# Optimization experiments

Measured on AMD Instinct MI355X. Metric: run time of the kernel, lower is better.

The kernel has to match this reference:

```python
import jax, jax.numpy as jnp
import numpy as np
from jax import lax

BCE_WEIGHT = 0.5
DICE_WEIGHT = 0.5
BOUNDARY_WEIGHT = 3.0
KERNEL_SIZE = 3
SMOOTH = 1e-6
EPS = 1e-7  # clamp for log stability (torch BCE clamps log at -100)


def setup_inputs() -> dict:
    key = jax.random.key(0)
    k1, k2 = jax.random.split(key)
    B, C, H, W = 32, 1, 512, 512
    pred = jax.random.uniform(k1, (B, C, H, W), dtype=jnp.float32)
    target = jax.random.randint(k2, (B, C, H, W), 0, 2, dtype=jnp.int32)
    return {"pred": pred, "target": target}


def _extract_boundary(t):
    # cv2 dilate/erode with all-ones 3x3 kernel == 3x3 max/min pooling.
    # cv2 morphology border behavior (-inf for dilate, +inf for erode)
    # matches reduce_window identity padding with 'SAME'.
    k = KERNEL_SIZE
    win = (1, 1, k, k)
    one = (1, 1, 1, 1)
    dilated = lax.reduce_window(t, -jnp.inf, lax.max, win, one, 'SAME')
    eroded = lax.reduce_window(t, jnp.inf, lax.min, win, one, 'SAME')
    return dilated - eroded  # in {0,1} for binary masks


def reference(pred, target):
    t = target.astype(jnp.float32)  # (B,1,H,W) binary

    # Boundary-aware weighted BCE
    boundary = _extract_boundary(t)
    weights = jnp.where(boundary > 0, BOUNDARY_WEIGHT, 1.0)
    p = jnp.clip(pred, EPS, 1.0 - EPS)
    bce_map = -(t * jnp.log(p) + (1.0 - t) * jnp.log1p(-p))
    bce = jnp.mean(bce_map * weights)

    # Dice loss over flattened tensors
    pf = pred.reshape(-1)
    tf = t.reshape(-1)
    intersection = jnp.sum(pf * tf)
    dice_coef = (2.0 * intersection + SMOOTH) / (jnp.sum(pf) + jnp.sum(tf) + SMOOTH)
    dice = 1.0 - dice_coef

    total = BCE_WEIGHT * bce + DICE_WEIGHT * dice
    return total, bce, dice
```

## Files before the change

### kernel.cpp

```cpp
#include <hip/hip_runtime.h>


#define BB 32
#define HH 512
#define WW 512
#define N_TOTAL (BB * HH * WW)
#define NBLK 2048

__global__ __launch_bounds__(256) void loss_main_kernel(
        const float* __restrict__ pred,
        const int* __restrict__ target,
        float4* __restrict__ partials) {
    const int wave = threadIdx.x >> 6;
    const int lane = threadIdx.x & 63;
    const int gw   = blockIdx.x * 4 + wave;
    const int b    = gw >> 8;
    const int h0   = (gw & 255) << 1;
    const int w0   = lane << 3;

    const size_t img = (size_t)b * (HH * WW);
    const int* tg   = target + img;
    const float* pg = pred + img;

    const int hm = (h0 > 0) ? h0 - 1 : 0;
    const int hp = (h0 + 2 < HH) ? h0 + 2 : HH - 1;

    const int4 r0A = *(const int4*)(tg + (size_t)hm * WW + w0);
    const int4 r0B = *(const int4*)(tg + (size_t)hm * WW + w0 + 4);
    const int4 r1A = *(const int4*)(tg + (size_t)h0 * WW + w0);
    const int4 r1B = *(const int4*)(tg + (size_t)h0 * WW + w0 + 4);
    const int4 r2A = *(const int4*)(tg + (size_t)(h0 + 1) * WW + w0);
    const int4 r2B = *(const int4*)(tg + (size_t)(h0 + 1) * WW + w0 + 4);
    const int4 r3A = *(const int4*)(tg + (size_t)hp * WW + w0);
    const int4 r3B = *(const int4*)(tg + (size_t)hp * WW + w0 + 4);

    const float4 pT0 = *(const float4*)(pg + (size_t)h0 * WW + w0);
    const float4 pT1 = *(const float4*)(pg + (size_t)h0 * WW + w0 + 4);
    const float4 pB0 = *(const float4*)(pg + (size_t)(h0 + 1) * WW + w0);
    const float4 pB1 = *(const float4*)(pg + (size_t)(h0 + 1) * WW + w0 + 4);

#define VC(i, u, c1, c2, d)                                          \
    const int so##i = (c1) | (c2), sa##i = (c1) & (c2);              \
    const int oT##i = so##i | (u), nT##i = sa##i & (u);              \
    const int oB##i = so##i | (d), nB##i = sa##i & (d);
    VC(0, r0A.x, r1A.x, r2A.x, r3A.x)
    VC(1, r0A.y, r1A.y, r2A.y, r3A.y)
    VC(2, r0A.z, r1A.z, r2A.z, r3A.z)
    VC(3, r0A.w, r1A.w, r2A.w, r3A.w)
    VC(4, r0B.x, r1B.x, r2B.x, r3B.x)
    VC(5, r0B.y, r1B.y, r2B.y, r3B.y)
    VC(6, r0B.z, r1B.z, r2B.z, r3B.z)
    VC(7, r0B.w, r1B.w, r2B.w, r3B.w)
#undef VC

    int oTL = __shfl_up(oT7, 1),   nTL = __shfl_up(nT7, 1);
    int oTR = __shfl_down(oT0, 1), nTR = __shfl_down(nT0, 1);
    int oBL = __shfl_up(oB7, 1),   nBL = __shfl_up(nB7, 1);
    int oBR = __shfl_down(oB0, 1), nBR = __shfl_down(nB0, 1);
    if (lane == 0)  { oTL = oT0; nTL = nT0; oBL = oB0; nBL = nB0; }
    if (lane == 63) { oTR = oT7; nTR = nT7; oBR = oB7; nBR = nB7; }

    const int eT0 = (oTL | oT0 | oT1) != (nTL & nT0 & nT1);
    const int eT1 = (oT0 | oT1 | oT2) != (nT0 & nT1 & nT2);
    const int eT2 = (oT1 | oT2 | oT3) != (nT1 & nT2 & nT3);
    const int eT3 = (oT2 | oT3 | oT4) != (nT2 & nT3 & nT4);
    const int eT4 = (oT3 | oT4 | oT5) != (nT3 & nT4 & nT5);
    const int eT5 = (oT4 | oT5 | oT6) != (nT4 & nT5 & nT6);
    const int eT6 = (oT5 | oT6 | oT7) != (nT5 & nT6 & nT7);
    const int eT7 = (oT6 | oT7 | oTR) != (nT6 & nT7 & nTR);
    const int eB0 = (oBL | oB0 | oB1) != (nBL & nB0 & nB1);
    const int eB1 = (oB0 | oB1 | oB2) != (nB0 & nB1 & nB2);
    const int eB2 = (oB1 | oB2 | oB3) != (nB1 & nB2 & nB3);
    const int eB3 = (oB2 | oB3 | oB4) != (nB2 & nB3 & nB4);
    const int eB4 = (oB3 | oB4 | oB5) != (nB3 & nB4 & nB5);
    const int eB5 = (oB4 | oB5 | oB6) != (nB4 & nB5 & nB6);
    const int eB6 = (oB5 | oB6 | oB7) != (nB5 & nB6 & nB7);
    const int eB7 = (oB6 | oB7 | oBR) != (nB6 & nB7 & nBR);

    float wbce = 0.f, inter = 0.f, sp = 0.f;
    int st_i = 0;

#define ACC(T, P, E)                                                   \
    {                                                                  \
        const float pc = fminf(fmaxf((P), 1e-7f), 1.0f - 1e-7f);       \
        const float x  = (T) ? pc : (1.0f - pc);                       \
        wbce += ((E) ? 3.0f : 1.0f) * (-__logf(x));                    \
        sp += (P);                                                     \
        if (T) inter += (P);                                           \
        st_i += (T);                                                   \
    }
    ACC(r1A.x, pT0.x, eT0); ACC(r1A.y, pT0.y, eT1);
    ACC(r1A.z, pT0.z, eT2); ACC(r1A.w, pT0.w, eT3);
    ACC(r1B.x, pT1.x, eT4); ACC(r1B.y, pT1.y, eT5);
    ACC(r1B.z, pT1.z, eT6); ACC(r1B.w, pT1.w, eT7);
    ACC(r2A.x, pB0.x, eB0); ACC(r2A.y, pB0.y, eB1);
    ACC(r2A.z, pB0.z, eB2); ACC(r2A.w, pB0.w, eB3);
    ACC(r2B.x, pB1.x, eB4); ACC(r2B.y, pB1.y, eB5);
    ACC(r2B.z, pB1.z, eB6); ACC(r2B.w, pB1.w, eB7);
#undef ACC

    float st = (float)st_i;
    #pragma unroll
    for (int off = 32; off > 0; off >>= 1) {
        wbce  += __shfl_down(wbce,  off);
        inter += __shfl_down(inter, off);
        sp    += __shfl_down(sp,    off);
        st    += __shfl_down(st,    off);
    }

    __shared__ float smem[4][4];
    if ((threadIdx.x & 63) == 0) {
        smem[wave][0] = wbce; smem[wave][1] = inter;
        smem[wave][2] = sp;   smem[wave][3] = st;
    }
    __syncthreads();
    if (threadIdx.x == 0) {
        float s0 = 0, s1 = 0, s2 = 0, s3 = 0;
        #pragma unroll
        for (int wv = 0; wv < 4; ++wv) {
            s0 += smem[wv][0]; s1 += smem[wv][1];
            s2 += smem[wv][2]; s3 += smem[wv][3];
        }
        partials[blockIdx.x] = make_float4(s0, s1, s2, s3);
    }
}

__global__ __launch_bounds__(1024) void finalize_kernel(
        const float4* __restrict__ partials, float* __restrict__ out) {
    double a0 = 0, a1 = 0, a2 = 0, a3 = 0;
    #pragma unroll
    for (int k = 0; k < NBLK / 1024; ++k) {
        const float4 p = partials[k * 1024 + threadIdx.x];
        a0 += p.x; a1 += p.y; a2 += p.z; a3 += p.w;
    }
    #pragma unroll
    for (int off = 32; off > 0; off >>= 1) {
        a0 += __shfl_down(a0, off);
        a1 += __shfl_down(a1, off);
        a2 += __shfl_down(a2, off);
        a3 += __shfl_down(a3, off);
    }
    __shared__ double smem[16][4];
    const int wave = threadIdx.x >> 6;
    if ((threadIdx.x & 63) == 0) {
        smem[wave][0] = a0; smem[wave][1] = a1;
        smem[wave][2] = a2; smem[wave][3] = a3;
    }
    __syncthreads();
    if (threadIdx.x == 0) {
        double s0 = 0, s1 = 0, s2 = 0, s3 = 0;
        #pragma unroll
        for (int wv = 0; wv < 16; ++wv) {
            s0 += smem[wv][0]; s1 += smem[wv][1];
            s2 += smem[wv][2]; s3 += smem[wv][3];
        }
        const double bce = s0 / (double)N_TOTAL;
        const double dice_coef = (2.0 * s1 + 1e-6) / (s2 + s3 + 1e-6);
        const double dice = 1.0 - dice_coef;
        const double total = 0.5 * bce + 0.5 * dice;
        out[0] = (float)total;
        out[1] = (float)bce;
        out[2] = (float)dice;
    }
}

extern "C" void kernel_launch(void* const* d_in, const int* in_sizes, int n_in,
                              void* d_out, int out_size, void* d_ws, size_t ws_size,
                              hipStream_t stream) {
    const float* pred  = (const float*)d_in[0];
    const int* target  = (const int*)d_in[1];
    float* out = (float*)d_out;
    float4* partials = (float4*)d_ws;

    loss_main_kernel<<<NBLK, 256, 0, stream>>>(pred, target, partials);
    finalize_kernel<<<1, 1024, 0, stream>>>(partials, out);
}
```

Baseline: 22.01 us.

## Process four rows per wave to cut target halo reloads and halve blocks

```diff
diff --git a/kernel.cpp b/kernel.cpp
--- a/kernel.cpp
+++ b/kernel.cpp
@@ -5,7 +5,7 @@
 #define HH 512
 #define WW 512
 #define N_TOTAL (BB * HH * WW)
-#define NBLK 2048
+#define NBLK 1024
 
 __global__ __launch_bounds__(256) void loss_main_kernel(
         const float* __restrict__ pred,
@@ -14,68 +14,38 @@
     const int wave = threadIdx.x >> 6;
     const int lane = threadIdx.x & 63;
     const int gw   = blockIdx.x * 4 + wave;
-    const int b    = gw >> 8;
-    const int h0   = (gw & 255) << 1;
+    const int b    = gw >> 7;
+    const int h0   = (gw & 127) << 2;
     const int w0   = lane << 3;
 
-    const size_t img = (size_t)b * (HH * WW);
+    const int img = b * (HH * WW);
     const int* tg   = target + img;
     const float* pg = pred + img;
 
     const int hm = (h0 > 0) ? h0 - 1 : 0;
-    const int hp = (h0 + 2 < HH) ? h0 + 2 : HH - 1;
+    const int hp = (h0 + 4 < HH) ? h0 + 4 : HH - 1;
 
-    const int4 r0A = *(const int4*)(tg + (size_t)hm * WW + w0);
-    const int4 r0B = *(const int4*)(tg + (size_t)hm * WW + w0 + 4);
-    const int4 r1A = *(const int4*)(tg + (size_t)h0 * WW + w0);
-    const int4 r1B = *(const int4*)(tg + (size_t)h0 * WW + w0 + 4);
-    const int4 r2A = *(const int4*)(tg + (size_t)(h0 + 1) * WW + w0);
-    const int4 r2B = *(const int4*)(tg + (size_t)(h0 + 1) * WW + w0 + 4);
-    const int4 r3A = *(const int4*)(tg + (size_t)hp * WW + w0);
-    const int4 r3B = *(const int4*)(tg + (size_t)hp * WW + w0 + 4);
+    const int4 r0A = *(const int4*)(tg + hm * WW + w0);
+    const int4 r0B = *(const int4*)(tg + hm * WW + w0 + 4);
+    const int4 r1A = *(const int4*)(tg + h0 * WW + w0);
+    const int4 r1B = *(const int4*)(tg + h0 * WW + w0 + 4);
+    const int4 r2A = *(const int4*)(tg + (h0 + 1) * WW + w0);
+    const int4 r2B = *(const int4*)(tg + (h0 + 1) * WW + w0 + 4);
+    const int4 r3A = *(const int4*)(tg + (h0 + 2) * WW + w0);
+    const int4 r3B = *(const int4*)(tg + (h0 + 2) * WW + w0 + 4);
+    const int4 r4A = *(const int4*)(tg + (h0 + 3) * WW + w0);
+    const int4 r4B = *(const int4*)(tg + (h0 + 3) * WW + w0 + 4);
+    const int4 r5A = *(const int4*)(tg + hp * WW + w0);
+    const int4 r5B = *(const int4*)(tg + hp * WW + w0 + 4);
 
-    const float4 pT0 = *(const float4*)(pg + (size_t)h0 * WW + w0);
-    const float4 pT1 = *(const float4*)(pg + (size_t)h0 * WW + w0 + 4);
-    const float4 pB0 = *(const float4*)(pg + (size_t)(h0 + 1) * WW + w0);
-    const float4 pB1 = *(const float4*)(pg + (size_t)(h0 + 1) * WW + w0 + 4);
-
-#define VC(i, u, c1, c2, d)                                          \
-    const int so##i = (c1) | (c2), sa##i = (c1) & (c2);              \
-    const int oT##i = so##i | (u), nT##i = sa##i & (u);              \
-    const int oB##i = so##i | (d), nB##i = sa##i & (d);
-    VC(0, r0A.x, r1A.x, r2A.x, r3A.x)
-    VC(1, r0A.y, r1A.y, r2A.y, r3A.y)
-    VC(2, r0A.z, r1A.z, r2A.z, r3A.z)
-    VC(3, r0A.w, r1A.w, r2A.w, r3A.w)
-    VC(4, r0B.x, r1B.x, r2B.x, r3B.x)
-    VC(5, r0B.y, r1B.y, r2B.y, r3B.y)
-    VC(6, r0B.z, r1B.z, r2B.z, r3B.z)
-    VC(7, r0B.w, r1B.w, r2B.w, r3B.w)
-#undef VC
-
-    int oTL = __shfl_up(oT7, 1),   nTL = __shfl_up(nT7, 1);
-    int oTR = __shfl_down(oT0, 1), nTR = __shfl_down(nT0, 1);
-    int oBL = __shfl_up(oB7, 1),   nBL = __shfl_up(nB7, 1);
-    int oBR = __shfl_down(oB0, 1), nBR = __shfl_down(nB0, 1);
-    if (lane == 0)  { oTL = oT0; nTL = nT0; oBL = oB0; nBL = nB0; }
-    if (lane == 63) { oTR = oT7; nTR = nT7; oBR = oB7; nBR = nB7; }
-
-    const int eT0 = (oTL | oT0 | oT1) != (nTL & nT0 & nT1);
-    const int eT1 = (oT0 | oT1 | oT2) != (nT0 & nT1 & nT2);
-    const int eT2 = (oT1 | oT2 | oT3) != (nT1 & nT2 & nT3);
-    const int eT3 = (oT2 | oT3 | oT4) != (nT2 & nT3 & nT4);
-    const int eT4 = (oT3 | oT4 | oT5) != (nT3 & nT4 & nT5);
-    const int eT5 = (oT4 | oT5 | oT6) != (nT4 & nT5 & nT6);
-    const int eT6 = (oT5 | oT6 | oT7) != (nT5 & nT6 & nT7);
-    const int eT7 = (oT6 | oT7 | oTR) != (nT6 & nT7 & nTR);
-    const int eB0 = (oBL | oB0 | oB1) != (nBL & nB0 & nB1);
-    const int eB1 = (oB0 | oB1 | oB2) != (nB0 & nB1 & nB2);
-    const int eB2 = (oB1 | oB2 | oB3) != (nB1 & nB2 & nB3);
-    const int eB3 = (oB2 | oB3 | oB4) != (nB2 & nB3 & nB4);
-    const int eB4 = (oB3 | oB4 | oB5) != (nB3 & nB4 & nB5);
-    const int eB5 = (oB4 | oB5 | oB6) != (nB4 & nB5 & nB6);
-    const int eB6 = (oB5 | oB6 | oB7) != (nB5 & nB6 & nB7);
-    const int eB7 = (oB6 | oB7 | oBR) != (nB6 & nB7 & nBR);
+    const float4 q0a = *(const float4*)(pg + h0 * WW + w0);
+    const float4 q0b = *(const float4*)(pg + h0 * WW + w0 + 4);
+    const float4 q1a = *(const float4*)(pg + (h0 + 1) * WW + w0);
+    const float4 q1b = *(const float4*)(pg + (h0 + 1) * WW + w0 + 4);
+    const float4 q2a = *(const float4*)(pg + (h0 + 2) * WW + w0);
+    const float4 q2b = *(const float4*)(pg + (h0 + 2) * WW + w0 + 4);
+    const float4 q3a = *(const float4*)(pg + (h0 + 3) * WW + w0);
+    const float4 q3b = *(const float4*)(pg + (h0 + 3) * WW + w0 + 4);
 
     float wbce = 0.f, inter = 0.f, sp = 0.f;
     int st_i = 0;
@@ -89,14 +59,40 @@
         if (T) inter += (P);                                           \
         st_i += (T);                                                   \
     }
-    ACC(r1A.x, pT0.x, eT0); ACC(r1A.y, pT0.y, eT1);
-    ACC(r1A.z, pT0.z, eT2); ACC(r1A.w, pT0.w, eT3);
-    ACC(r1B.x, pT1.x, eT4); ACC(r1B.y, pT1.y, eT5);
-    ACC(r1B.z, pT1.z, eT6); ACC(r1B.w, pT1.w, eT7);
-    ACC(r2A.x, pB0.x, eB0); ACC(r2A.y, pB0.y, eB1);
-    ACC(r2A.z, pB0.z, eB2); ACC(r2A.w, pB0.w, eB3);
-    ACC(r2B.x, pB1.x, eB4); ACC(r2B.y, pB1.y, eB5);
-    ACC(r2B.z, pB1.z, eB6); ACC(r2B.w, pB1.w, eB7);
+
+#define DOROW(uA, uB, cA, cB, dA, dB, P0, P1)                               \
+    {                                                                       \
+        const int o0 = uA.x | cA.x | dA.x,  n0 = uA.x & cA.x & dA.x;        \
+        const int o1 = uA.y | cA.y | dA.y,  n1 = uA.y & cA.y & dA.y;        \
+        const int o2 = uA.z | cA.z | dA.z,  n2 = uA.z & cA.z & dA.z;        \
+        const int o3 = uA.w | cA.w | dA.w,  n3 = uA.w & cA.w & dA.w;        \
+        const int o4 = uB.x | cB.x | dB.x,  n4 = uB.x & cB.x & dB.x;        \
+        const int o5 = uB.y | cB.y | dB.y,  n5 = uB.y & cB.y & dB.y;        \
+        const int o6 = uB.z | cB.z | dB.z,  n6 = uB.z & cB.z & dB.z;        \
+        const int o7 = uB.w | cB.w | dB.w,  n7 = uB.w & cB.w & dB.w;        \
+        int oL = __shfl_up(o7, 1),   nL = __shfl_up(n7, 1);                 \
+        int oR = __shfl_down(o0, 1), nR = __shfl_down(n0, 1);               \
+        if (lane == 0)  { oL = o0; nL = n0; }                               \
+        if (lane == 63) { oR = o7; nR = n7; }                               \
+        const int e0 = (oL | o0 | o1) != (nL & n0 & n1);                    \
+        const int e1 = (o0 | o1 | o2) != (n0 & n1 & n2);                    \
+        const int e2 = (o1 | o2 | o3) != (n1 & n2 & n3);                    \
+        const int e3 = (o2 | o3 | o4) != (n2 & n3 & n4);                    \
+        const int e4 = (o3 | o4 | o5) != (n3 & n4 & n5);                    \
+        const int e5 = (o4 | o5 | o6) != (n4 & n5 & n6);                    \
+        const int e6 = (o5 | o6 | o7) != (n5 & n6 & n7);                    \
+        const int e7 = (o6 | o7 | oR) != (n6 & n7 & nR);                    \
+        ACC(cA.x, P0.x, e0); ACC(cA.y, P0.y, e1);                           \
+        ACC(cA.z, P0.z, e2); ACC(cA.w, P0.w, e3);                           \
+        ACC(cB.x, P1.x, e4); ACC(cB.y, P1.y, e5);                           \
+        ACC(cB.z, P1.z, e6); ACC(cB.w, P1.w, e7);                           \
+    }
+
+    DOROW(r0A, r0B, r1A, r1B, r2A, r2B, q0a, q0b)
+    DOROW(r1A, r1B, r2A, r2B, r3A, r3B, q1a, q1b)
+    DOROW(r2A, r2B, r3A, r3B, r4A, r4B, q2a, q2b)
+    DOROW(r3A, r3B, r4A, r4B, r5A, r5B, q3a, q3b)
+#undef DOROW
 #undef ACC
 
     float st = (float)st_i;
@@ -127,12 +123,8 @@
 
 __global__ __launch_bounds__(1024) void finalize_kernel(
         const float4* __restrict__ partials, float* __restrict__ out) {
-    double a0 = 0, a1 = 0, a2 = 0, a3 = 0;
-    #pragma unroll
-    for (int k = 0; k < NBLK / 1024; ++k) {
-        const float4 p = partials[k * 1024 + threadIdx.x];
-        a0 += p.x; a1 += p.y; a2 += p.z; a3 += p.w;
-    }
+    const float4 p = partials[threadIdx.x];
+    double a0 = p.x, a1 = p.y, a2 = p.z, a3 = p.w;
     #pragma unroll
     for (int off = 32; off > 0; off >>= 1) {
         a0 += __shfl_down(a0, off);
```

After: 23.45 us. 1.07x slower.

## Fuse finalize into main kernel via hierarchical last-block atomic counters

Applied to the files above, without the earlier changes.

```diff
diff --git a/kernel.cpp b/kernel.cpp
--- a/kernel.cpp
+++ b/kernel.cpp
@@ -6,11 +6,14 @@
 #define WW 512
 #define N_TOTAL (BB * HH * WW)
 #define NBLK 2048
+#define SUBT 32
+#define PER_SUB (NBLK / SUBT)
 
 __global__ __launch_bounds__(256) void loss_main_kernel(
         const float* __restrict__ pred,
         const int* __restrict__ target,
-        float4* __restrict__ partials) {
+        char* __restrict__ ws,
+        float* __restrict__ out) {
     const int wave = threadIdx.x >> 6;
     const int lane = threadIdx.x & 63;
     const int gw   = blockIdx.x * 4 + wave;
@@ -108,13 +111,19 @@
         st    += __shfl_down(st,    off);
     }
 
+    float4* partials  = (float4*)(ws + 8192);
+    unsigned* sub     = (unsigned*)(ws + (size_t)(blockIdx.x & (SUBT - 1)) * 128);
+    unsigned* superT  = (unsigned*)(ws + 4096);
+
     __shared__ float smem[4][4];
+    __shared__ int is_last;
     if ((threadIdx.x & 63) == 0) {
         smem[wave][0] = wbce; smem[wave][1] = inter;
         smem[wave][2] = sp;   smem[wave][3] = st;
     }
     __syncthreads();
     if (threadIdx.x == 0) {
+        is_last = 0;
         float s0 = 0, s1 = 0, s2 = 0, s3 = 0;
         #pragma unroll
         for (int wv = 0; wv < 4; ++wv) {
@@ -122,45 +131,52 @@
             s2 += smem[wv][2]; s3 += smem[wv][3];
         }
         partials[blockIdx.x] = make_float4(s0, s1, s2, s3);
-    }
-}
-
-__global__ __launch_bounds__(1024) void finalize_kernel(
-        const float4* __restrict__ partials, float* __restrict__ out) {
-    double a0 = 0, a1 = 0, a2 = 0, a3 = 0;
-    #pragma unroll
-    for (int k = 0; k < NBLK / 1024; ++k) {
-        const float4 p = partials[k * 1024 + threadIdx.x];
-        a0 += p.x; a1 += p.y; a2 += p.z; a3 += p.w;
-    }
-    #pragma unroll
-    for (int off = 32; off > 0; off >>= 1) {
-        a0 += __shfl_down(a0, off);
-        a1 += __shfl_down(a1, off);
-        a2 += __shfl_down(a2, off);
-        a3 += __shfl_down(a3, off);
-    }
-    __shared__ double smem[16][4];
-    const int wave = threadIdx.x >> 6;
-    if ((threadIdx.x & 63) == 0) {
-        smem[wave][0] = a0; smem[wave][1] = a1;
-        smem[wave][2] = a2; smem[wave][3] = a3;
+        __threadfence();
+        const unsigned o = atomicAdd(sub, 1u);
+        if (o == PER_SUB - 1) {
+            const unsigned o2 = atomicAdd(superT, 1u);
+            if (o2 == SUBT - 1) is_last = 1;
+        }
     }
     __syncthreads();
-    if (threadIdx.x == 0) {
-        double s0 = 0, s1 = 0, s2 = 0, s3 = 0;
+
+    if (is_last) {
+        double a0 = 0, a1 = 0, a2 = 0, a3 = 0;
+        for (int k = threadIdx.x; k < NBLK; k += 256) {
+            const float* p = (const float*)&partials[k];
+            a0 += __hip_atomic_load(p + 0, __ATOMIC_RELAXED, __HIP_MEMORY_SCOPE_AGENT);
+            a1 += __hip_atomic_load(p + 1, __ATOMIC_RELAXED, __HIP_MEMORY_SCOPE_AGENT);
+            a2 += __hip_atomic_load(p + 2, __ATOMIC_RELAXED, __HIP_MEMORY_SCOPE_AGENT);
+            a3 += __hip_atomic_load(p + 3, __ATOMIC_RELAXED, __HIP_MEMORY_SCOPE_AGENT);
+        }
         #pragma unroll
-        for (int wv = 0; wv < 16; ++wv) {
-            s0 += smem[wv][0]; s1 += smem[wv][1];
-            s2 += smem[wv][2]; s3 += smem[wv][3];
+        for (int off = 32; off > 0; off >>= 1) {
+            a0 += __shfl_down(a0, off);
+            a1 += __shfl_down(a1, off);
+            a2 += __shfl_down(a2, off);
+            a3 += __shfl_down(a3, off);
         }
-        const double bce = s0 / (double)N_TOTAL;
-        const double dice_coef = (2.0 * s1 + 1e-6) / (s2 + s3 + 1e-6);
-        const double dice = 1.0 - dice_coef;
-        const double total = 0.5 * bce + 0.5 * dice;
-        out[0] = (float)total;
-        out[1] = (float)bce;
-        out[2] = (float)dice;
+        __shared__ double dmem[4][4];
+        if ((threadIdx.x & 63) == 0) {
+            dmem[wave][0] = a0; dmem[wave][1] = a1;
+            dmem[wave][2] = a2; dmem[wave][3] = a3;
+        }
+        __syncthreads();
+        if (threadIdx.x == 0) {
+            double s0 = 0, s1 = 0, s2 = 0, s3 = 0;
+            #pragma unroll
+            for (int wv = 0; wv < 4; ++wv) {
+                s0 += dmem[wv][0]; s1 += dmem[wv][1];
+                s2 += dmem[wv][2]; s3 += dmem[wv][3];
+            }
+            const double bce = s0 / (double)N_TOTAL;
+            const double dice_coef = (2.0 * s1 + 1e-6) / (s2 + s3 + 1e-6);
+            const double dice = 1.0 - dice_coef;
+            const double total = 0.5 * bce + 0.5 * dice;
+            out[0] = (float)total;
+            out[1] = (float)bce;
+            out[2] = (float)dice;
+        }
     }
 }
 
@@ -170,8 +186,8 @@
     const float* pred  = (const float*)d_in[0];
     const int* target  = (const int*)d_in[1];
     float* out = (float*)d_out;
-    float4* partials = (float4*)d_ws;
+    char* ws = (char*)d_ws;
 
-    loss_main_kernel<<<NBLK, 256, 0, stream>>>(pred, target, partials);
-    finalize_kernel<<<1, 1024, 0, stream>>>(partials, out);
+    hipMemsetAsync(ws, 0, 8192, stream);
+    loss_main_kernel<<<NBLK, 256, 0, stream>>>(pred, target, ws, out);
 }
```

After: 87.24 us. 296% more time.
